# Kernel tuning notes

Measured on AMD Instinct MI355X. Metric: run time of the kernel, lower is better.

Reference implementation:

```python
import jax, jax.numpy as jnp
import numpy as np

GAMMA = 0.99
RHO_THRESHOLD = 1.0
C_THRESHOLD = 1.0
BASELINE_LOSS_SCALING = 0.5
ENT_COEFF = 0.01
PPO_CLIP = 0.2


def setup_inputs() -> dict:
    key = jax.random.key(0)
    ks = jax.random.split(key, 7)
    T, B, A = 512, 8192, 2
    return {
        "prob": jax.random.uniform(ks[0], (T, B, A), dtype=jnp.float32),
        "action_prob": jax.random.uniform(ks[1], (T, B, A), dtype=jnp.float32),
        "v": jax.random.normal(ks[2], (T, B), dtype=jnp.float32),
        "next_v": jax.random.normal(ks[3], (T, B), dtype=jnp.float32),
        "reward": jax.random.normal(ks[4], (T, B), dtype=jnp.float32),
        "action": jax.random.randint(ks[5], (T, B), 0, 2, dtype=jnp.int32),
        "done": jax.random.randint(ks[6], (T, B), 0, 2, dtype=jnp.int32),
    }


def _log_prob(p, a):
    # torch.distributions.Categorical normalizes unnormalized probs
    logp = jnp.log(p) - jnp.log(p.sum(-1, keepdims=True))  # [T,B,A]
    return jnp.take_along_axis(logp, a[..., None].astype(jnp.int32), axis=-1)[..., 0]


def reference(prob, action_prob, v, next_v, reward, action, done):
    done_f = done.astype(v.dtype)  # [T,B]
    logp = _log_prob(prob, action)
    logp_act = _log_prob(action_prob, action)
    ratio = jnp.exp(logp - logp_act)  # [T,B]

    clipped_rho = jnp.minimum(ratio, RHO_THRESHOLD)
    clipped_c = jnp.minimum(ratio, C_THRESHOLD)
    deltas = clipped_rho * (reward + (1.0 - done_f) * GAMMA * next_v - v)

    # V-trace backward recurrence over time (dim 0), vectorized over batch
    def step(next_vtrace, xs):
        v_t, d_t, c_t, rho_t, r_t, nv_t, dn_t = xs
        vt = v_t + d_t + GAMMA * c_t * (next_vtrace - nv_t) * (1.0 - dn_t)
        adv = rho_t * (r_t + GAMMA * next_vtrace * (1.0 - dn_t) - v_t)
        return vt, (vt, adv)

    _, (vtrace, adv) = jax.lax.scan(
        step, next_v[-1],
        (v, deltas, clipped_c, clipped_rho, reward, next_v, done_f),
        reverse=True)

    vtrace = jax.lax.stop_gradient(vtrace)  # .detach() in original
    adv = jax.lax.stop_gradient(adv)

    critic_loss = BASELINE_LOSS_SCALING * jnp.mean((v - vtrace) ** 2)
    surr1 = ratio * adv
    surr2 = jnp.clip(ratio, 1.0 - PPO_CLIP, 1.0 + PPO_CLIP) * adv
    actor_loss = -jnp.minimum(surr1, surr2).mean()

    # entropy is logged but NOT included in total_loss in the original
    total_loss = actor_loss + critic_loss
    return total_loss
```

## Files before the change

### kernel.cpp

```cpp
#include <hip/hip_runtime.h>

#define T_DIM 512
#define B_DIM 8192
#define GB 16
#define NC 64
#define LC 8
#define GAMMA 0.99f

__launch_bounds__(1024, 8)
__global__ void vtrace_main(const float* __restrict__ prob,
                            const float* __restrict__ aprob,
                            const float* __restrict__ v,
                            const float* __restrict__ nv,
                            const float* __restrict__ rw,
                            const int* __restrict__ act,
                            const int* __restrict__ dnn,
                            float* __restrict__ partials) {
    __shared__ float Sc[NC][GB];
    __shared__ float Mc[NC][GB];
    __shared__ float Cin[NC][GB];
    __shared__ float red[32];

    const int tid = threadIdx.x;
    const int bl  = tid & (GB - 1);
    const int c   = tid >> 4;
    const int swz = (blockIdx.x & 7) * (512 / 8) + (blockIdx.x >> 3);
    const int b   = swz * GB + bl;
    const int t0  = c * LC;

    float S = 0.0f, M = 1.0f;
    float r0,r1,r2,r3,r4,r5,r6,r7;
    float p0,p1,p2,p3,p4,p5,p6,p7;
    float w0,w1,w2,w3,w4,w5,w6,w7;

    const float2* __restrict__ prob2  = (const float2*)prob;
    const float2* __restrict__ aprob2 = (const float2*)aprob;
    const size_t base = (size_t)t0 * B_DIM + b;

#define STEPA(i)                                                            \
    {                                                                       \
        const size_t idx = base + (size_t)(i) * B_DIM;                      \
        float2 pr = prob2[idx];                                             \
        float2 qr = aprob2[idx];                                            \
        float vvi = v[idx];                                                 \
        float rr  = rw[idx];                                                \
        int   a   = act[idx];                                               \
        int   d   = dnn[idx];                                               \
        float pa    = a ? pr.y : pr.x;                                      \
        float qa    = a ? qr.y : qr.x;                                      \
        float ratio = (pa * (qr.x + qr.y)) / ((pr.x + pr.y) * qa);          \
        float rho   = fminf(ratio, 1.0f);                                   \
        float m     = d ? 0.0f : GAMMA * rho;                               \
        float p     = rho * (rr - vvi);                                     \
        r##i = __uint_as_float(__float_as_uint(ratio) |                     \
                               ((unsigned)d << 31));                        \
        p##i = p;                                                           \
        w##i = vvi;                                                         \
        S = (vvi + p) + m * S;                                              \
        M = m * M;                                                          \
    }

    STEPA(7) STEPA(6) STEPA(5) STEPA(4) STEPA(3) STEPA(2) STEPA(1) STEPA(0)
#undef STEPA

    Sc[c][bl] = S;
    Mc[c][bl] = M;
    __syncthreads();

    if (tid < GB) {
        float carry = nv[(size_t)(T_DIM - 1) * B_DIM + swz * GB + tid];
#pragma unroll 8
        for (int cc = NC - 1; cc >= 0; --cc) {
            Cin[cc][tid] = carry;
            carry = fmaf(Mc[cc][tid], carry, Sc[cc][tid]);
        }
    }
    __syncthreads();

    float carry  = Cin[c][bl];
    float critic = 0.0f, msum = 0.0f;

#define STEPB(i)                                                            \
    {                                                                       \
        const unsigned u  = __float_as_uint(r##i);                          \
        const float r_    = __uint_as_float(u & 0x7fffffffu);               \
        const float m     = ((int)u < 0) ? 0.0f : GAMMA * fminf(r_, 1.0f);  \
        const float adv   = fmaf(m, carry, p##i);                           \
        carry = w##i + adv;                                                 \
        critic = fmaf(adv, adv, critic);                                    \
        msum += (adv >= 0.0f) ? fminf(r_, 1.2f) * adv                       \
                              : fmaxf(r_, 0.8f) * adv;                      \
    }

    STEPB(7) STEPB(6) STEPB(5) STEPB(4) STEPB(3) STEPB(2) STEPB(1) STEPB(0)
#undef STEPB

#pragma unroll
    for (int off = 32; off > 0; off >>= 1) {
        critic += __shfl_down(critic, off, 64);
        msum   += __shfl_down(msum, off, 64);
    }
    const int wave = tid >> 6;
    if ((tid & 63) == 0) { red[wave] = critic; red[16 + wave] = msum; }
    __syncthreads();
    if (tid == 0) {
        float cs = 0.0f, ms = 0.0f;
#pragma unroll
        for (int w = 0; w < 16; ++w) { cs += red[w]; ms += red[16 + w]; }
        partials[swz]       = cs;
        partials[512 + swz] = ms;
    }
}

__global__ void vtrace_final(const float* __restrict__ partials,
                             float* __restrict__ out) {
    __shared__ float red[16];
    const int tid = threadIdx.x;
    float cs = partials[tid];
    float ms = partials[512 + tid];
#pragma unroll
    for (int off = 32; off > 0; off >>= 1) {
        cs += __shfl_down(cs, off, 64);
        ms += __shfl_down(ms, off, 64);
    }
    const int wave = tid >> 6;
    if ((tid & 63) == 0) { red[wave] = cs; red[8 + wave] = ms; }
    __syncthreads();
    if (tid == 0) {
        float c = 0.0f, m = 0.0f;
#pragma unroll
        for (int w = 0; w < 8; ++w) { c += red[w]; m += red[8 + w]; }
        const float invN = 1.0f / (float)((size_t)T_DIM * B_DIM);
        out[0] = 0.5f * c * invN - m * invN;
    }
}

extern "C" void kernel_launch(void* const* d_in, const int* in_sizes, int n_in,
                              void* d_out, int out_size, void* d_ws, size_t ws_size,
                              hipStream_t stream) {
    const float* prob  = (const float*)d_in[0];
    const float* aprob = (const float*)d_in[1];
    const float* v     = (const float*)d_in[2];
    const float* nv    = (const float*)d_in[3];
    const float* rw    = (const float*)d_in[4];
    const int*   act   = (const int*)d_in[5];
    const int*   dnn   = (const int*)d_in[6];
    float* partials = (float*)d_ws;
    float* out      = (float*)d_out;

    vtrace_main<<<B_DIM / GB, GB * NC, 0, stream>>>(prob, aprob, v, nv, rw,
                                                    act, dnn, partials);
    vtrace_final<<<1, 512, 0, stream>>>(partials, out);
}
```

Baseline: 177.2 us.

## Use cooperative grid-sync kernel with time slabs and global carry propagation

Replaces the per-block chunked scan with a cooperative kernel where each block handles a 16-step time slab across 1024 batch columns. Slab summaries go to global workspace, a grid sync runs a serial carry pass over 32 slabs in 8 blocks, and a second sync is followed by the final pass. Ratios are kept in LDS, while v and reward are re-read from global memory. The aim is coalesced wide-row loads and more parallelism in time, at the cost of two grid syncs, a serialized carry phase and re-reads. The old kernel stays as a fallback when the workspace is too small.

```diff
diff --git a/kernel.cpp b/kernel.cpp
--- a/kernel.cpp
+++ b/kernel.cpp
@@ -1,100 +1,191 @@
 #include <hip/hip_runtime.h>
+#include <hip/hip_cooperative_groups.h>
+
+namespace cg = cooperative_groups;
 
 #define T_DIM 512
 #define B_DIM 8192
-#define GB 16
-#define NC 64
-#define LC 8
+#define SLT   16
+#define NSLAB (T_DIM / SLT)
+#define GC    1024
+#define NCG   (B_DIM / GC)
+#define NTH   1024
+#define NBLK  (NSLAB * NCG)
 #define GAMMA 0.99f
 
-__launch_bounds__(1024, 8)
-__global__ void vtrace_main(const float* __restrict__ prob,
-                            const float* __restrict__ aprob,
-                            const float* __restrict__ v,
-                            const float* __restrict__ nv,
-                            const float* __restrict__ rw,
-                            const int* __restrict__ act,
-                            const int* __restrict__ dnn,
-                            float* __restrict__ partials) {
-    __shared__ float Sc[NC][GB];
-    __shared__ float Mc[NC][GB];
-    __shared__ float Cin[NC][GB];
+#define WS_S    0
+#define WS_M    (NSLAB * B_DIM)
+#define WS_CIN  (2 * NSLAB * B_DIM)
+#define WS_PART (3 * NSLAB * B_DIM)
+#define WS_NEED_BYTES ((size_t)(WS_PART + 2 * NBLK) * sizeof(float))
+
+__global__ __launch_bounds__(NTH)
+void vtrace_coop(const float* __restrict__ prob,
+                 const float* __restrict__ aprob,
+                 const float* __restrict__ v,
+                 const float* __restrict__ nv,
+                 const float* __restrict__ rw,
+                 const int* __restrict__ act,
+                 const int* __restrict__ dnn,
+                 float* __restrict__ ws) {
+    __shared__ unsigned int rs[SLT][NTH];
     __shared__ float red[32];
 
+    cg::grid_group grid = cg::this_grid();
+
     const int tid = threadIdx.x;
-    const int bl  = tid & (GB - 1);
-    const int c   = tid >> 4;
-    const int swz = (blockIdx.x & 7) * (512 / 8) + (blockIdx.x >> 3);
-    const int b   = swz * GB + bl;
-    const int t0  = c * LC;
-
-    float S = 0.0f, M = 1.0f;
-    float r0,r1,r2,r3,r4,r5,r6,r7;
-    float p0,p1,p2,p3,p4,p5,p6,p7;
-    float w0,w1,w2,w3,w4,w5,w6,w7;
+    const int bid = blockIdx.x;
+    const int s   = bid >> 3;
+    const int g   = bid & (NCG - 1);
+    const int col = g * GC + tid;
+    const int t0  = s * SLT;
 
     const float2* __restrict__ prob2  = (const float2*)prob;
     const float2* __restrict__ aprob2 = (const float2*)aprob;
-    const size_t base = (size_t)t0 * B_DIM + b;
-
+
+    float S = 0.0f, M = 1.0f;
+#pragma unroll
+    for (int i = SLT - 1; i >= 0; --i) {
+        const size_t idx = (size_t)(t0 + i) * B_DIM + col;
+        const float2 pr = prob2[idx];
+        const float2 qr = aprob2[idx];
+        const float  vv = v[idx];
+        const float  rr = rw[idx];
+        const int    a  = act[idx];
+        const int    d  = dnn[idx];
+
+        const float pa    = a ? pr.y : pr.x;
+        const float qa    = a ? qr.y : qr.x;
+        const float ratio = (pa * (qr.x + qr.y)) / ((pr.x + pr.y) * qa);
+        const float rho   = fminf(ratio, 1.0f);
+        const float m     = d ? 0.0f : GAMMA * rho;
+        const float p     = rho * (rr - vv);
+
+        rs[i][tid] = __float_as_uint(ratio) | ((unsigned)d << 31);
+        S = (vv + p) + m * S;
+        M = m * M;
+    }
+    ws[WS_S + s * B_DIM + col] = S;
+    ws[WS_M + s * B_DIM + col] = M;
+
+    grid.sync();
+
+    if (bid < NCG) {
+        const int c2 = bid * NTH + tid;
+        float carry = nv[(size_t)(T_DIM - 1) * B_DIM + c2];
+#pragma unroll
+        for (int ss = NSLAB - 1; ss >= 0; --ss) {
+            ws[WS_CIN + ss * B_DIM + c2] = carry;
+            carry = fmaf(ws[WS_M + ss * B_DIM + c2], carry,
+                         ws[WS_S + ss * B_DIM + c2]);
+        }
+    }
+
+    grid.sync();
+
+    float carry  = ws[WS_CIN + s * B_DIM + col];
+    float critic = 0.0f, msum = 0.0f;
+#pragma unroll
+    for (int i = SLT - 1; i >= 0; --i) {
+        const size_t idx = (size_t)(t0 + i) * B_DIM + col;
+        const float vv = v[idx];
+        const float rr = rw[idx];
+        const unsigned u = rs[i][tid];
+
+        const float r_  = __uint_as_float(u & 0x7fffffffu);
+        const float m   = ((int)u < 0) ? 0.0f : GAMMA * fminf(r_, 1.0f);
+        const float p   = fminf(r_, 1.0f) * (rr - vv);
+        const float t_  = m * carry;
+        const float adv = p + t_;
+        carry = (vv + p) + t_;
+        critic = fmaf(adv, adv, critic);
+        msum += (adv >= 0.0f) ? fminf(r_, 1.2f) * adv
+                              : fmaxf(r_, 0.8f) * adv;
+    }
+
+#pragma unroll
+    for (int off = 32; off > 0; off >>= 1) {
+        critic += __shfl_down(critic, off, 64);
+        msum   += __shfl_down(msum, off, 64);
+    }
+    const int wave = tid >> 6;
+    if ((tid & 63) == 0) { red[wave] = critic; red[16 + wave] = msum; }
+    __syncthreads();
+    if (tid == 0) {
+        float cs = 0.0f, ms = 0.0f;
+#pragma unroll
+        for (int w = 0; w < 16; ++w) { cs += red[w]; ms += red[16 + w]; }
+        ws[WS_PART + bid]        = cs;
+        ws[WS_PART + NBLK + bid] = ms;
+    }
+}
+
+#define GB_FB 16
+#define NC_FB 64
+#define LC_FB 8
+__global__ __launch_bounds__(1024)
+void vtrace_fb(const float* __restrict__ prob, const float* __restrict__ aprob,
+               const float* __restrict__ v, const float* __restrict__ nv,
+               const float* __restrict__ rw, const int* __restrict__ act,
+               const int* __restrict__ dnn, float* __restrict__ partials) {
+    __shared__ float Sc[NC_FB][GB_FB];
+    __shared__ float Mc[NC_FB][GB_FB];
+    __shared__ float Cin[NC_FB][GB_FB];
+    __shared__ float red[32];
+    const int tid = threadIdx.x;
+    const int bl  = tid & (GB_FB - 1);
+    const int c   = tid >> 4;
+    const int b   = blockIdx.x * GB_FB + bl;
+    const float2* __restrict__ prob2  = (const float2*)prob;
+    const float2* __restrict__ aprob2 = (const float2*)aprob;
+    const size_t base = (size_t)(c * LC_FB) * B_DIM + b;
+    float S = 0.0f, M = 1.0f;
+    float r0,r1,r2,r3,r4,r5,r6,r7, p0,p1,p2,p3,p4,p5,p6,p7,
+          w0,w1,w2,w3,w4,w5,w6,w7;
 #define STEPA(i)                                                            \
     {                                                                       \
         const size_t idx = base + (size_t)(i) * B_DIM;                      \
-        float2 pr = prob2[idx];                                             \
-        float2 qr = aprob2[idx];                                            \
-        float vvi = v[idx];                                                 \
-        float rr  = rw[idx];                                                \
-        int   a   = act[idx];                                               \
-        int   d   = dnn[idx];                                               \
-        float pa    = a ? pr.y : pr.x;                                      \
-        float qa    = a ? qr.y : qr.x;                                      \
+        float2 pr = prob2[idx]; float2 qr = aprob2[idx];                    \
+        float vvi = v[idx]; float rr = rw[idx];                             \
+        int a = act[idx]; int d = dnn[idx];                                 \
+        float pa = a ? pr.y : pr.x; float qa = a ? qr.y : qr.x;             \
         float ratio = (pa * (qr.x + qr.y)) / ((pr.x + pr.y) * qa);          \
-        float rho   = fminf(ratio, 1.0f);                                   \
-        float m     = d ? 0.0f : GAMMA * rho;                               \
-        float p     = rho * (rr - vvi);                                     \
+        float rho = fminf(ratio, 1.0f);                                     \
+        float m = d ? 0.0f : GAMMA * rho;                                   \
+        float p = rho * (rr - vvi);                                         \
         r##i = __uint_as_float(__float_as_uint(ratio) |                     \
                                ((unsigned)d << 31));                        \
-        p##i = p;                                                           \
-        w##i = vvi;                                                         \
-        S = (vvi + p) + m * S;                                              \
-        M = m * M;                                                          \
-    }
-
+        p##i = p; w##i = vvi;                                               \
+        S = (vvi + p) + m * S; M = m * M;                                   \
+    }
     STEPA(7) STEPA(6) STEPA(5) STEPA(4) STEPA(3) STEPA(2) STEPA(1) STEPA(0)
 #undef STEPA
-
-    Sc[c][bl] = S;
-    Mc[c][bl] = M;
-    __syncthreads();
-
-    if (tid < GB) {
-        float carry = nv[(size_t)(T_DIM - 1) * B_DIM + swz * GB + tid];
+    Sc[c][bl] = S; Mc[c][bl] = M;
+    __syncthreads();
+    if (tid < GB_FB) {
+        float carry = nv[(size_t)(T_DIM - 1) * B_DIM + blockIdx.x * GB_FB + tid];
 #pragma unroll 8
-        for (int cc = NC - 1; cc >= 0; --cc) {
+        for (int cc = NC_FB - 1; cc >= 0; --cc) {
             Cin[cc][tid] = carry;
             carry = fmaf(Mc[cc][tid], carry, Sc[cc][tid]);
         }
     }
     __syncthreads();
-
-    float carry  = Cin[c][bl];
+    float carry = Cin[c][bl];
     float critic = 0.0f, msum = 0.0f;
-
 #define STEPB(i)                                                            \
     {                                                                       \
-        const unsigned u  = __float_as_uint(r##i);                          \
-        const float r_    = __uint_as_float(u & 0x7fffffffu);               \
-        const float m     = ((int)u < 0) ? 0.0f : GAMMA * fminf(r_, 1.0f);  \
-        const float adv   = fmaf(m, carry, p##i);                           \
+        const unsigned u = __float_as_uint(r##i);                           \
+        const float r_ = __uint_as_float(u & 0x7fffffffu);                  \
+        const float m = ((int)u < 0) ? 0.0f : GAMMA * fminf(r_, 1.0f);      \
+        const float adv = fmaf(m, carry, p##i);                             \
         carry = w##i + adv;                                                 \
         critic = fmaf(adv, adv, critic);                                    \
         msum += (adv >= 0.0f) ? fminf(r_, 1.2f) * adv                       \
                               : fmaxf(r_, 0.8f) * adv;                      \
     }
-
     STEPB(7) STEPB(6) STEPB(5) STEPB(4) STEPB(3) STEPB(2) STEPB(1) STEPB(0)
 #undef STEPB
-
 #pragma unroll
     for (int off = 32; off > 0; off >>= 1) {
         critic += __shfl_down(critic, off, 64);
@@ -107,17 +198,17 @@
         float cs = 0.0f, ms = 0.0f;
 #pragma unroll
         for (int w = 0; w < 16; ++w) { cs += red[w]; ms += red[16 + w]; }
-        partials[swz]       = cs;
-        partials[512 + swz] = ms;
-    }
-}
-
-__global__ void vtrace_final(const float* __restrict__ partials,
+        partials[blockIdx.x]       = cs;
+        partials[512 + blockIdx.x] = ms;
+    }
+}
+
+__global__ void vtrace_final(const float* __restrict__ partials, int n,
                              float* __restrict__ out) {
     __shared__ float red[16];
     const int tid = threadIdx.x;
-    float cs = partials[tid];
-    float ms = partials[512 + tid];
+    float cs = (tid < n) ? partials[tid] : 0.0f;
+    float ms = (tid < n) ? partials[n + tid] : 0.0f;
 #pragma unroll
     for (int off = 32; off > 0; off >>= 1) {
         cs += __shfl_down(cs, off, 64);
@@ -145,10 +236,18 @@
     const float* rw    = (const float*)d_in[4];
     const int*   act   = (const int*)d_in[5];
     const int*   dnn   = (const int*)d_in[6];
-    float* partials = (float*)d_ws;
-    float* out      = (float*)d_out;
-
-    vtrace_main<<<B_DIM / GB, GB * NC, 0, stream>>>(prob, aprob, v, nv, rw,
-                                                    act, dnn, partials);
-    vtrace_final<<<1, 512, 0, stream>>>(partials, out);
-}
+    float* ws  = (float*)d_ws;
+    float* out = (float*)d_out;
+
+    if (ws_size >= WS_NEED_BYTES) {
+        void* args[] = {(void*)&prob, (void*)&aprob, (void*)&v, (void*)&nv,
+                        (void*)&rw, (void*)&act, (void*)&dnn, (void*)&ws};
+        hipLaunchCooperativeKernel((void*)vtrace_coop, dim3(NBLK), dim3(NTH),
+                                   args, 0, stream);
+        vtrace_final<<<1, 512, 0, stream>>>(ws + WS_PART, NBLK, out);
+    } else {
+        vtrace_fb<<<B_DIM / GB_FB, 1024, 0, stream>>>(prob, aprob, v, nv, rw,
+                                                      act, dnn, ws);
+        vtrace_final<<<1, 512, 0, stream>>>(ws, 512, out);
+    }
+}
```

After: 263.3 us. 48.6% more time.
